# Optimization experiments

Measured on AMD Instinct MI355X. Metric: run time of the kernel, lower is better.

Reference implementation:

```python
import jax, jax.numpy as jnp
import numpy as np
from jax import lax

VOCAB, EMB, H, L, B = 32000, 512, 512, 256, 64


def _flip_bwd(t):
    # t: (L, B, 2, ...); reverse time for the backward direction (dir index 1)
    return jnp.stack([t[:, :, 0], t[::-1, :, 1]], axis=2)


def sru_layer(x, W, bias, k, n_out):
    """Bidirectional SRU layer.
    x: (L, B, n_in); W: (n_in, 2*n_out*k); bias: (2, 2, n_out) = (gate{f,r}, dir, n_out).
    k=4: 4th projection is the highway input; k=3: highway uses x itself (n_in == 2*n_out).
    """
    Lx, Bx, _ = x.shape
    u = (x @ W).reshape(Lx, Bx, 2, n_out, k)
    u = _flip_bwd(u)  # both directions now scan forward in time
    f = jax.nn.sigmoid(u[..., 1] + bias[0][None, None])  # (L,B,2,n_out)
    r = jax.nn.sigmoid(u[..., 2] + bias[1][None, None])
    x_tilde = u[..., 0]

    def step(c, inp):
        f_t, xt = inp
        c = f_t * c + (1.0 - f_t) * xt
        return c, c

    c0 = jnp.zeros((Bx, 2, n_out), x.dtype)
    c_last, cs = lax.scan(step, c0, (f, x_tilde))

    if k == 4:
        x_res = u[..., 3]
    else:
        x_res = _flip_bwd(x.reshape(Lx, Bx, 2, n_out))
    h = r * jnp.tanh(cs) + (1.0 - r) * x_res
    h = _flip_bwd(h)  # restore true time order for backward dir
    return h.reshape(Lx, Bx, 2 * n_out), c_last.reshape(Bx, 2 * n_out)


def setup_inputs() -> dict:
    key = jax.random.key(0)
    ks = jax.random.split(key, 8)
    inp = {
        'padded_encoder_inputs': jax.random.randint(ks[0], (L, B), 0, VOCAB),
        'emb': jax.random.normal(ks[1], (VOCAB, EMB), jnp.float32) * 0.1,
        'W0': jax.random.normal(ks[2], (EMB, 2 * H * 4), jnp.float32) * 0.05,
        'b0': jax.random.normal(ks[3], (2, 2, H), jnp.float32) * 0.05,
        'W1': jax.random.normal(ks[4], (2 * H, 2 * H * 3), jnp.float32) * 0.05,
        'b1': jax.random.normal(ks[5], (2, 2, H), jnp.float32) * 0.05,
        'Wd': jax.random.normal(ks[6], (H, 2 * H), jnp.float32) * 0.05,
        'bd': jax.random.normal(ks[7], (H,), jnp.float32) * 0.05,
    }
    return inp


def reference(padded_encoder_inputs, emb, W0, b0, W1, b1, Wd, bd):
    # embedding lookup (dropout layers are identity in eval mode)
    x = emb[padded_encoder_inputs]            # (L, B, EMB)
    h1, c1 = sru_layer(x, W0, b0, 4, H)       # (L,B,2H), (B,2H)
    h2, c2 = sru_layer(h1, W1, b1, 3, H)
    hidden = jnp.stack([c1, c2], axis=0)      # (layers, B, 2H)
    hidden = hidden @ Wd.T + bd               # dense_hidden: (layers, B, H)
    return h2, hidden
```

## Files before the change

### kernel.cpp

```cpp
#include <hip/hip_runtime.h>

typedef __attribute__((ext_vector_type(8))) short bf16x8;
typedef __attribute__((ext_vector_type(4))) float f32x4;

__device__ __forceinline__ float b2f(ushort s) { return __uint_as_float(((uint)s) << 16); }
__device__ __forceinline__ ushort f2b(float f) {
  uint u = __float_as_uint(f);
  u += 0x7fff + ((u >> 16) & 1);
  return (ushort)(u >> 16);
}

__device__ __forceinline__ void store_h(float* p, float v) { *p = v; }
__device__ __forceinline__ void store_h(ushort* p, float v) { *p = f2b(v); }

__device__ __forceinline__ float sigm_fast(float x) { return 1.f / (1.f + __expf(-x)); }
__device__ __forceinline__ float tanh_fast(float c) {
  float e = __expf(-2.f * fabsf(c));
  float t = (1.f - e) / (1.f + e);
  return copysignf(t, c);
}

__global__ void transpose_kernel(const float* __restrict__ in, ushort* __restrict__ out,
                                 int R, int C) {
  __shared__ ushort tile[32][33];
  int bc = blockIdx.x << 5;
  int br = blockIdx.y << 5;
  int tx = threadIdx.x & 31;
  int ty = threadIdx.x >> 5;
#pragma unroll
  for (int i = 0; i < 32; i += 8)
    tile[ty + i][tx] = f2b(in[(size_t)(br + ty + i) * C + bc + tx]);
  __syncthreads();
#pragma unroll
  for (int i = 0; i < 32; i += 8)
    out[(size_t)(bc + ty + i) * R + br + tx] = tile[tx][ty + i];
}

__global__ void embed_kernel(const int* __restrict__ tok, const float* __restrict__ emb,
                             ushort* __restrict__ x) {
  int tid = threadIdx.x;
  int r = (blockIdx.x << 2) + (tid >> 6);
  int c = (tid & 63) << 3;
  int t = tok[r];
  const float* src = emb + ((size_t)t << 9) + c;
  float4 a = *(const float4*)src;
  float4 b = *(const float4*)(src + 4);
  uint4 o;
  o.x = (uint)f2b(a.x) | ((uint)f2b(a.y) << 16);
  o.y = (uint)f2b(a.z) | ((uint)f2b(a.w) << 16);
  o.z = (uint)f2b(b.x) | ((uint)f2b(b.y) << 16);
  o.w = (uint)f2b(b.z) | ((uint)f2b(b.w) << 16);
  *(uint4*)(x + ((size_t)r << 9) + c) = o;
}

__global__ __launch_bounds__(256) void gemm_bt_kernel(
    const ushort* __restrict__ A, const ushort* __restrict__ BT,
    ushort* __restrict__ C, int M, int N, int K) {
  __shared__ ushort As[128 * 64];
  __shared__ ushort Bs[128 * 64];
  const int tid = threadIdx.x;
  const int lane = tid & 63;
  const int wave = tid >> 6;
  const int wm = (wave >> 1) << 6;
  const int wn = (wave & 1) << 6;
  const int m0 = blockIdx.x << 7;
  const int n0 = blockIdx.y << 7;

  f32x4 acc[4][4];
#pragma unroll
  for (int i = 0; i < 4; ++i)
#pragma unroll
    for (int j = 0; j < 4; ++j) acc[i][j] = (f32x4){0.f, 0.f, 0.f, 0.f};

  const int wbase = wave << 12;
  for (int k0 = 0; k0 < K; k0 += 64) {
#pragma unroll
    for (int i = 0; i < 4; ++i) {
      int p = wbase + (i << 10) + (lane << 4);
      int row = p >> 7;
      int col = ((p & 127) ^ ((row & 7) << 4)) >> 1;
      const ushort* ga = A + (size_t)(m0 + row) * K + k0 + col;
      const ushort* gb = BT + (size_t)(n0 + row) * K + k0 + col;
      __builtin_amdgcn_global_load_lds(
          (const __attribute__((address_space(1))) void*)ga,
          (__attribute__((address_space(3))) void*)((char*)As + wbase + (i << 10)), 16, 0, 0);
      __builtin_amdgcn_global_load_lds(
          (const __attribute__((address_space(1))) void*)gb,
          (__attribute__((address_space(3))) void*)((char*)Bs + wbase + (i << 10)), 16, 0, 0);
    }
    __syncthreads();
#pragma unroll
    for (int kk = 0; kk < 2; ++kk) {
      const int kof = (kk << 5) + ((lane >> 4) << 3);
      bf16x8 af[4], bg[4];
#pragma unroll
      for (int mi = 0; mi < 4; ++mi) {
        int row = wm + (mi << 4) + (lane & 15);
        int byte = ((row << 6) + kof) * 2;
        byte ^= (row & 7) << 4;
        af[mi] = *(const bf16x8*)((const char*)As + byte);
      }
#pragma unroll
      for (int ni = 0; ni < 4; ++ni) {
        int row = wn + (ni << 4) + (lane & 15);
        int byte = ((row << 6) + kof) * 2;
        byte ^= (row & 7) << 4;
        bg[ni] = *(const bf16x8*)((const char*)Bs + byte);
      }
#pragma unroll
      for (int mi = 0; mi < 4; ++mi)
#pragma unroll
        for (int ni = 0; ni < 4; ++ni)
          acc[mi][ni] =
              __builtin_amdgcn_mfma_f32_16x16x32_bf16(af[mi], bg[ni], acc[mi][ni], 0, 0, 0);
    }
    __syncthreads();
  }
#pragma unroll
  for (int mi = 0; mi < 4; ++mi) {
#pragma unroll
    for (int j = 0; j < 4; ++j) {
      int row = m0 + wm + (mi << 4) + ((lane >> 4) << 2) + j;
      size_t base = (size_t)row * N + n0 + wn;
#pragma unroll
      for (int ni = 0; ni < 4; ++ni)
        C[base + (ni << 4) + (lane & 15)] = f2b(acc[mi][ni][j]);
    }
  }
}

template <int KC, typename OT>
__global__ void sru_scan_kernel(const ushort* __restrict__ u, const float* __restrict__ bias,
                                const ushort* __restrict__ xres, OT* __restrict__ hout,
                                float* __restrict__ cout) {
  const int L = 256, B = 64, H = 512;
  int idx = blockIdx.x * 256 + threadIdx.x;
  int h = idx & (H - 1);
  int dir = (idx >> 9) & 1;
  int b = idx >> 10;
  float bfg = bias[dir * H + h];
  float brg = bias[2 * H + dir * H + h];
  const size_t ustep = (size_t)B * 2 * H * KC;
  const ushort* ubase = u + ((size_t)b * 2 + dir) * H * KC + (size_t)h * KC;
  const size_t hstep = (size_t)B * 2 * H;
  const size_t hoff = (size_t)b * 2 * H + (size_t)dir * H + h;
  float c = 0.f;
#pragma unroll 16
  for (int s = 0; s < L; ++s) {
    int t = dir ? (L - 1 - s) : s;
    const ushort* up = ubase + (size_t)t * ustep;
    float xt, fg, rg, xr;
    if (KC == 4) {
      uint2 v = *(const uint2*)up;
      xt = b2f((ushort)(v.x & 0xffff));
      fg = b2f((ushort)(v.x >> 16));
      rg = b2f((ushort)(v.y & 0xffff));
      xr = b2f((ushort)(v.y >> 16));
    } else {
      xt = b2f(up[0]);
      fg = b2f(up[1]);
      rg = b2f(up[2]);
      xr = b2f(xres[hoff + (size_t)t * hstep]);
    }
    float f = sigm_fast(fg + bfg);
    float r = sigm_fast(rg + brg);
    c = f * c + (1.f - f) * xt;
    float hv = r * tanh_fast(c) + (1.f - r) * xr;
    store_h(hout + hoff + (size_t)t * hstep, hv);
  }
  cout[(size_t)b * 2 * H + (size_t)dir * H + h] = c;
}

__global__ __launch_bounds__(512) void dense_kernel(
    const float* __restrict__ c12, const ushort* __restrict__ WdT,
    const float* __restrict__ bd, float* __restrict__ out) {
  int row = blockIdx.x;
  int j = threadIdx.x;
  const float* c = c12 + (size_t)row * 1024;
  float acc = bd[j];
#pragma unroll 8
  for (int k = 0; k < 1024; ++k) acc += c[k] * b2f(WdT[(size_t)k * 512 + j]);
  out[(size_t)row * 512 + j] = acc;
}

extern "C" void kernel_launch(void* const* d_in, const int* in_sizes, int n_in,
                              void* d_out, int out_size, void* d_ws, size_t ws_size,
                              hipStream_t stream) {
  const int* tok = (const int*)d_in[0];
  const float* emb = (const float*)d_in[1];
  const float* W0 = (const float*)d_in[2];
  const float* b0 = (const float*)d_in[3];
  const float* W1 = (const float*)d_in[4];
  const float* b1 = (const float*)d_in[5];
  const float* Wd = (const float*)d_in[6];
  const float* bd = (const float*)d_in[7];
  float* out = (float*)d_out;

  char* ws = (char*)d_ws;
  ushort* x = (ushort*)ws;
  ushort* W0T = (ushort*)(ws + 16777216);
  ushort* W1T = (ushort*)(ws + 20971520);
  ushort* u = (ushort*)(ws + 27262976);
  ushort* h1 = (ushort*)(ws + 161480704);
  float* c12 = (float*)(ws + 195035136);
  ushort* WdT = (ushort*)(ws + 27262976 + 100663296);

  transpose_kernel<<<dim3(128, 16), 256, 0, stream>>>(W0, W0T, 512, 4096);
  transpose_kernel<<<dim3(96, 32), 256, 0, stream>>>(W1, W1T, 1024, 3072);
  embed_kernel<<<4096, 256, 0, stream>>>(tok, emb, x);
  gemm_bt_kernel<<<dim3(128, 32), 256, 0, stream>>>(x, W0T, u, 16384, 4096, 512);
  sru_scan_kernel<4, ushort><<<256, 256, 0, stream>>>(u, b0, (const ushort*)nullptr, h1, c12);
  gemm_bt_kernel<<<dim3(128, 24), 256, 0, stream>>>(h1, W1T, u, 16384, 3072, 1024);
  sru_scan_kernel<3, float><<<256, 256, 0, stream>>>(u, b1, h1, out, c12 + 65536);
  transpose_kernel<<<dim3(32, 16), 256, 0, stream>>>(Wd, WdT, 512, 1024);
  dense_kernel<<<128, 512, 0, stream>>>(c12, WdT, bd, out + 16777216);
}
```

Baseline: 394.6 us.

## Rewrite bf16 GEMM with triple-buffered LDS pipeline and larger tiles

```diff
diff --git a/kernel.cpp b/kernel.cpp
--- a/kernel.cpp
+++ b/kernel.cpp
@@ -53,78 +53,100 @@
   *(uint4*)(x + ((size_t)r << 9) + c) = o;
 }
 
-__global__ __launch_bounds__(256) void gemm_bt_kernel(
+__global__ __launch_bounds__(512) void gemm_bt2_kernel(
     const ushort* __restrict__ A, const ushort* __restrict__ BT,
-    ushort* __restrict__ C, int M, int N, int K) {
-  __shared__ ushort As[128 * 64];
-  __shared__ ushort Bs[128 * 64];
+    ushort* __restrict__ C, int M, int N, int K, int MT) {
+  __shared__ ushort lds[3][24576];
   const int tid = threadIdx.x;
   const int lane = tid & 63;
   const int wave = tid >> 6;
-  const int wm = (wave >> 1) << 6;
-  const int wn = (wave & 1) << 6;
-  const int m0 = blockIdx.x << 7;
-  const int n0 = blockIdx.y << 7;
-
-  f32x4 acc[4][4];
-#pragma unroll
-  for (int i = 0; i < 4; ++i)
-#pragma unroll
-    for (int j = 0; j < 4; ++j) acc[i][j] = (f32x4){0.f, 0.f, 0.f, 0.f};
-
-  const int wbase = wave << 12;
-  for (int k0 = 0; k0 < K; k0 += 64) {
-#pragma unroll
-    for (int i = 0; i < 4; ++i) {
-      int p = wbase + (i << 10) + (lane << 4);
-      int row = p >> 7;
-      int col = ((p & 127) ^ ((row & 7) << 4)) >> 1;
-      const ushort* ga = A + (size_t)(m0 + row) * K + k0 + col;
-      const ushort* gb = BT + (size_t)(n0 + row) * K + k0 + col;
+  const int wr = wave >> 2;
+  const int wc = wave & 3;
+
+  int q = gridDim.x >> 3;
+  int wg = (blockIdx.x & 7) * q + (blockIdx.x >> 3);
+  int mt = wg % MT;
+  int nt = wg / MT;
+  const int m0 = mt << 8;
+  const int n0 = nt << 7;
+  const int NT = K >> 6;
+
+  auto stage = [&](int t, int p) {
+    const ushort* Asrc = A + (size_t)m0 * K + (t << 6);
+    const ushort* Bsrc = BT + (size_t)n0 * K + (t << 6);
+    char* base = (char*)lds[p];
+#pragma unroll
+    for (int i = 0; i < 6; ++i) {
+      int sub = (i < 4) ? i : (i - 4);
+      int off = (sub << 13) + (tid << 4);
+      int row = off >> 7;
+      int col = ((off & 127) ^ ((row & 7) << 4)) >> 1;
+      const ushort* src = ((i < 4) ? Asrc : Bsrc) + (size_t)row * K + col;
+      char* dst = base + ((i < 4) ? 0 : 32768) + (sub << 13) + (wave << 10);
       __builtin_amdgcn_global_load_lds(
-          (const __attribute__((address_space(1))) void*)ga,
-          (__attribute__((address_space(3))) void*)((char*)As + wbase + (i << 10)), 16, 0, 0);
-      __builtin_amdgcn_global_load_lds(
-          (const __attribute__((address_space(1))) void*)gb,
-          (__attribute__((address_space(3))) void*)((char*)Bs + wbase + (i << 10)), 16, 0, 0);
-    }
-    __syncthreads();
+          (const __attribute__((address_space(1))) void*)src,
+          (__attribute__((address_space(3))) void*)dst, 16, 0, 0);
+    }
+  };
+
+  f32x4 acc[8][2];
+#pragma unroll
+  for (int i = 0; i < 8; ++i) {
+    acc[i][0] = (f32x4){0.f, 0.f, 0.f, 0.f};
+    acc[i][1] = (f32x4){0.f, 0.f, 0.f, 0.f};
+  }
+
+  stage(0, 0);
+  stage(1, 1);
+  for (int t = 0; t < NT; ++t) {
+    int p = t % 3;
+    if (t + 1 < NT) {
+      asm volatile("s_waitcnt vmcnt(6)" ::: "memory");
+    } else {
+      asm volatile("s_waitcnt vmcnt(0)" ::: "memory");
+    }
+    __builtin_amdgcn_s_barrier();
+    __builtin_amdgcn_sched_barrier(0);
+    if (t + 2 < NT) stage(t + 2, (t + 2) % 3);
+    __builtin_amdgcn_sched_barrier(0);
+    const char* base = (const char*)lds[p];
 #pragma unroll
     for (int kk = 0; kk < 2; ++kk) {
-      const int kof = (kk << 5) + ((lane >> 4) << 3);
-      bf16x8 af[4], bg[4];
-#pragma unroll
-      for (int mi = 0; mi < 4; ++mi) {
-        int row = wm + (mi << 4) + (lane & 15);
-        int byte = ((row << 6) + kof) * 2;
+      const int kof2 = ((kk << 5) + ((lane >> 4) << 3)) << 1;
+      bf16x8 af[8], bg[2];
+#pragma unroll
+      for (int mi = 0; mi < 8; ++mi) {
+        int row = (wr << 7) + (mi << 4) + (lane & 15);
+        int byte = (row << 7) + kof2;
         byte ^= (row & 7) << 4;
-        af[mi] = *(const bf16x8*)((const char*)As + byte);
+        af[mi] = *(const bf16x8*)(base + byte);
       }
 #pragma unroll
-      for (int ni = 0; ni < 4; ++ni) {
-        int row = wn + (ni << 4) + (lane & 15);
-        int byte = ((row << 6) + kof) * 2;
+      for (int ni = 0; ni < 2; ++ni) {
+        int row = (wc << 5) + (ni << 4) + (lane & 15);
+        int byte = (row << 7) + kof2;
         byte ^= (row & 7) << 4;
-        bg[ni] = *(const bf16x8*)((const char*)Bs + byte);
+        bg[ni] = *(const bf16x8*)(base + 32768 + byte);
       }
-#pragma unroll
-      for (int mi = 0; mi < 4; ++mi)
-#pragma unroll
-        for (int ni = 0; ni < 4; ++ni)
+      __builtin_amdgcn_s_setprio(1);
+#pragma unroll
+      for (int mi = 0; mi < 8; ++mi)
+#pragma unroll
+        for (int ni = 0; ni < 2; ++ni)
           acc[mi][ni] =
               __builtin_amdgcn_mfma_f32_16x16x32_bf16(af[mi], bg[ni], acc[mi][ni], 0, 0, 0);
-    }
-    __syncthreads();
-  }
-#pragma unroll
-  for (int mi = 0; mi < 4; ++mi) {
+      __builtin_amdgcn_s_setprio(0);
+    }
+  }
+#pragma unroll
+  for (int mi = 0; mi < 8; ++mi) {
 #pragma unroll
     for (int j = 0; j < 4; ++j) {
-      int row = m0 + wm + (mi << 4) + ((lane >> 4) << 2) + j;
-      size_t base = (size_t)row * N + n0 + wn;
-#pragma unroll
-      for (int ni = 0; ni < 4; ++ni)
-        C[base + (ni << 4) + (lane & 15)] = f2b(acc[mi][ni][j]);
+      int row = m0 + (wr << 7) + (mi << 4) + ((lane >> 4) << 2) + j;
+      size_t bofs = (size_t)row * N + n0 + (wc << 5);
+#pragma unroll
+      for (int ni = 0; ni < 2; ++ni)
+        C[bofs + (ni << 4) + (lane & 15)] = f2b(acc[mi][ni][j]);
     }
   }
 }
@@ -208,9 +230,9 @@
   transpose_kernel<<<dim3(128, 16), 256, 0, stream>>>(W0, W0T, 512, 4096);
   transpose_kernel<<<dim3(96, 32), 256, 0, stream>>>(W1, W1T, 1024, 3072);
   embed_kernel<<<4096, 256, 0, stream>>>(tok, emb, x);
-  gemm_bt_kernel<<<dim3(128, 32), 256, 0, stream>>>(x, W0T, u, 16384, 4096, 512);
+  gemm_bt2_kernel<<<2048, 512, 0, stream>>>(x, W0T, u, 16384, 4096, 512, 64);
   sru_scan_kernel<4, ushort><<<256, 256, 0, stream>>>(u, b0, (const ushort*)nullptr, h1, c12);
-  gemm_bt_kernel<<<dim3(128, 24), 256, 0, stream>>>(h1, W1T, u, 16384, 3072, 1024);
+  gemm_bt2_kernel<<<1536, 512, 0, stream>>>(h1, W1T, u, 16384, 3072, 1024, 64);
   sru_scan_kernel<3, float><<<256, 256, 0, stream>>>(u, b1, h1, out, c12 + 65536);
   transpose_kernel<<<dim3(32, 16), 256, 0, stream>>>(Wd, WdT, 512, 1024);
   dense_kernel<<<128, 512, 0, stream>>>(c12, WdT, bd, out + 16777216);
```

Result: slower. 448.5 us (+13.6%).
